# Kernel tuning notes

Hardware: AMD Instinct MI355X
Metric: run time of the kernel (lower is better)

Reference implementation:

```python
import jax, jax.numpy as jnp
import numpy as np

V, E, HID, D = 10000, 512, 512, 14
FEAT = 512  # attention feature dim (== C)


def setup_inputs() -> dict:
    key = jax.random.key(0)
    ks = jax.random.split(key, 20)
    s = 0.02
    inp = {
        "features": jax.random.normal(ks[0], (32, 512, 7, 7), jnp.float32),
        "captions": jax.random.randint(ks[1], (32, 60), 0, V),
        "disease": jax.random.uniform(ks[2], (32, D), jnp.float32),
        # embedding
        "emb": jax.random.normal(ks[3], (V, E), jnp.float32) * s,
        # attention: attn Linear(feat+hid -> hid), v Linear(hid -> 1)
        "W_attn": jax.random.normal(ks[4], (FEAT + HID, HID), jnp.float32) * s,
        "b_attn": jnp.zeros((HID,), jnp.float32),
        "W_v": jax.random.normal(ks[5], (HID, 1), jnp.float32) * s,
        "b_v": jnp.zeros((1,), jnp.float32),
        # attention disease_proj: 14->128->512
        "W_dp1": jax.random.normal(ks[6], (D, 128), jnp.float32) * s,
        "b_dp1": jnp.zeros((128,), jnp.float32),
        "W_dp2": jax.random.normal(ks[7], (128, HID), jnp.float32) * s,
        "b_dp2": jnp.zeros((HID,), jnp.float32),
        # disease_encoder: 14->128->256 (dropout = identity at eval)
        "W_de1": jax.random.normal(ks[8], (D, 128), jnp.float32) * s,
        "b_de1": jnp.zeros((128,), jnp.float32),
        "W_de2": jax.random.normal(ks[9], (128, 256), jnp.float32) * s,
        "b_de2": jnp.zeros((256,), jnp.float32),
        # LSTM (input = E + 512 + 256 = 1280), gate order i,f,g,o
        "W_ih": jax.random.normal(ks[10], (E + FEAT + 256, 4 * HID), jnp.float32) * s,
        "W_hh": jax.random.normal(ks[11], (HID, 4 * HID), jnp.float32) * s,
        "b_ih": jnp.zeros((4 * HID,), jnp.float32),
        "b_hh": jnp.zeros((4 * HID,), jnp.float32),
        # fc: hid -> vocab
        "W_fc": jax.random.normal(ks[12], (HID, V), jnp.float32) * s,
        "b_fc": jnp.zeros((V,), jnp.float32),
    }
    return inp


def reference(features, captions, disease, emb, W_attn, b_attn, W_v, b_v,
              W_dp1, b_dp1, W_dp2, b_dp2, W_de1, b_de1, W_de2, b_de2,
              W_ih, W_hh, b_ih, b_hh, W_fc, b_fc):
    B, C = features.shape[0], features.shape[1]
    f = features.reshape(B, C, -1).transpose(0, 2, 1)  # [B, N, 512]

    embs = emb[captions]  # [B, T, E]

    # time-invariant disease contexts
    dis_ctx = jax.nn.relu(disease @ W_de1 + b_de1) @ W_de2 + b_de2   # [B,256]
    dis_att = jax.nn.relu(disease @ W_dp1 + b_dp1) @ W_dp2 + b_dp2  # [B,HID]

    # split attn weight: energy = tanh(f@Wf + (h+dis_att)@Wh + b)
    Wf, Wh = W_attn[:FEAT], W_attn[FEAT:]
    f_proj = jnp.einsum('bnf,fh->bnh', f, Wf)  # precompute feature part

    def step(carry, emb_t):
        h, c = carry  # [B,HID] each
        hid = h + dis_att
        energy = jnp.tanh(f_proj + (hid @ Wh + b_attn)[:, None, :])  # [B,N,HID]
        scores = (energy @ W_v).squeeze(-1) + b_v[0]                 # [B,N]
        alpha = jax.nn.softmax(scores, axis=1)
        context = jnp.einsum('bn,bnf->bf', alpha, f)                 # [B,512]
        x = jnp.concatenate([emb_t, context, dis_ctx], axis=1)       # [B,1280]
        gates = x @ W_ih + h @ W_hh + b_ih + b_hh
        i, fg, g, o = jnp.split(gates, 4, axis=1)
        c_new = jax.nn.sigmoid(fg) * c + jax.nn.sigmoid(i) * jnp.tanh(g)
        h_new = jax.nn.sigmoid(o) * jnp.tanh(c_new)
        return (h_new, c_new), h_new

    h0 = jnp.zeros((B, HID), f.dtype)
    c0 = jnp.zeros((B, HID), f.dtype)
    _, h_seq = jax.lax.scan(step, (h0, c0), embs.transpose(1, 0, 2))  # [T,B,HID]

    logits = h_seq @ W_fc + b_fc          # [T,B,V]
    return logits.transpose(1, 0, 2)      # [B,T,V]
```

## Files before the change

### kernel.cpp

```cpp
#include <hip/hip_runtime.h>
#include <math.h>

#define BB 32
#define NP 49
#define FE 512
#define HI 512
#define EM 512
#define TT 60
#define G4 2048
#define NV 10000
#define ND 14
#define NBLK 80

typedef __attribute__((ext_vector_type(8))) short short8v;
typedef __attribute__((ext_vector_type(4))) float float4v;

__device__ __forceinline__ float fsig(float x){ return 1.0f/(1.0f+__expf(-x)); }
__device__ __forceinline__ float ftanh(float x){
    x = fminf(fmaxf(x, -15.0f), 15.0f);
    float e = __expf(2.0f*x);
    return (e-1.0f)/(e+1.0f);
}
__device__ __forceinline__ ushort f2bf(float x){
    union { float f; unsigned u; } v; v.f = x;
    unsigned r = v.u + 0x7fff + ((v.u >> 16) & 1);
    return (ushort)(r >> 16);
}
__device__ __forceinline__ float bf2f(ushort h){
    union { float f; unsigned u; } v; v.u = ((unsigned)h) << 16;
    return v.f;
}
__device__ __forceinline__ ushort f2bf_trunc(float x){
    return (ushort)(__float_as_uint(x) >> 16);
}

__global__ void k_transpose(const float* __restrict__ feat, float* __restrict__ fT){
    int b = blockIdx.y;
    int cb = blockIdx.x * 64;
    __shared__ float tile[64][NP+1];
    const float* src = feat + (size_t)b*FE*NP;
    for (int idx = threadIdx.x; idx < 64*NP; idx += 256){
        int cl = idx / NP, n = idx % NP;
        tile[cl][n] = src[(size_t)(cb+cl)*NP + n];
    }
    __syncthreads();
    float* dst = fT + (size_t)b*NP*FE;
    for (int idx = threadIdx.x; idx < 64*NP; idx += 256){
        int cl = idx % 64, n = idx / 64;
        dst[(size_t)n*FE + cb + cl] = tile[cl][n];
    }
}

__global__ void k_disease(const float* __restrict__ dis,
                          const float* __restrict__ Wdp1, const float* __restrict__ bdp1,
                          const float* __restrict__ Wdp2, const float* __restrict__ bdp2,
                          const float* __restrict__ Wde1, const float* __restrict__ bde1,
                          const float* __restrict__ Wde2, const float* __restrict__ bde2,
                          const float* __restrict__ Wattn, const float* __restrict__ battn,
                          const float* __restrict__ Wih, const float* __restrict__ bih,
                          const float* __restrict__ bhh,
                          float* __restrict__ daw, float* __restrict__ disWih){
    int b = blockIdx.x;
    int tid = threadIdx.x;
    __shared__ float d[ND];
    __shared__ float hp[128], he[128];
    __shared__ float datt[HI];
    __shared__ float dctx[256];
    if (tid < ND) d[tid] = dis[b*ND + tid];
    __syncthreads();
    if (tid < 128){
        float accP = bdp1[tid], accE = bde1[tid];
        for (int k=0;k<ND;k++){ accP += d[k]*Wdp1[k*128+tid]; accE += d[k]*Wde1[k*128+tid]; }
        hp[tid] = fmaxf(accP, 0.f);
        he[tid] = fmaxf(accE, 0.f);
    }
    __syncthreads();
    for (int j = tid; j < HI; j += 256){
        float a = bdp2[j];
        for (int k=0;k<128;k++) a += hp[k]*Wdp2[k*HI+j];
        datt[j] = a;
    }
    if (tid < 256){
        float a = bde2[tid];
        for (int k=0;k<128;k++) a += he[k]*Wde2[k*256+tid];
        dctx[tid] = a;
    }
    __syncthreads();
    for (int j = tid; j < HI; j += 256){
        float a = battn[j];
        for (int k=0;k<HI;k++) a += datt[k]*Wattn[(size_t)(FE+k)*HI + j];
        daw[b*HI + j] = a;
    }
    for (int j = tid; j < G4; j += 256){
        float a = bih[j] + bhh[j];
        for (int k=0;k<256;k++) a += dctx[k]*Wih[(size_t)(EM+FE+k)*G4 + j];
        disWih[b*G4 + j] = a;
    }
}

__device__ __forceinline__ void stage_rows32(const float* __restrict__ src0, size_t ldsrc,
                                             const int* __restrict__ rowmap,
                                             ushort* h_hi, ushort* h_lo, int tid){
    #pragma unroll
    for (int it = 0; it < 4; it++){
        int flat = (it*512 + tid)*8;
        int row = flat >> 9, k = flat & 511;
        const float* src = src0 + (rowmap ? (size_t)rowmap[row]*ldsrc : (size_t)row*ldsrc) + k;
        float4 v0 = *(const float4*)(src);
        float4 v1 = *(const float4*)(src + 4);
        float fv[8] = {v0.x,v0.y,v0.z,v0.w,v1.x,v1.y,v1.z,v1.w};
        union { ushort u[8]; uint4 v; } ph, pl;
        #pragma unroll
        for (int j = 0; j < 8; j++){
            ushort hi = f2bf(fv[j]);
            ph.u[j] = hi;
            pl.u[j] = f2bf_trunc(fv[j] - bf2f(hi));
        }
        int di = (row*512 + k) ^ ((row&7)<<3);
        *(uint4*)&h_hi[di] = ph.v;
        *(uint4*)&h_lo[di] = pl.v;
    }
}

__device__ __forceinline__ void mfma_32x32(const ushort* h_hi, const ushort* h_lo,
                                           const float* __restrict__ Wb, size_t ldB, int col0,
                                           int lane, float4v acc[2][2]){
    int m = lane & 15, kg = lane >> 4;
    int a0 = m*512 + kg*8;
    int a1 = (16+m)*512 + kg*8;
    int axr = (m&7)<<3;
    for (int ks = 0; ks < 16; ks++){
        short8v ah0 = *(const short8v*)&h_hi[(a0 + ks*32) ^ axr];
        short8v al0 = *(const short8v*)&h_lo[(a0 + ks*32) ^ axr];
        short8v ah1 = *(const short8v*)&h_hi[(a1 + ks*32) ^ axr];
        short8v al1 = *(const short8v*)&h_lo[(a1 + ks*32) ^ axr];
        #pragma unroll
        for (int cj = 0; cj < 2; cj++){
            int v = col0 + cj*16 + m;
            int k0 = ks*32 + kg*8;
            const float* wp = Wb + (size_t)k0*ldB + v;
            float w[8];
            #pragma unroll
            for (int i = 0; i < 8; i++) w[i] = wp[(size_t)i*ldB];
            union { ushort u[8]; short8v s; } bh, bl;
            #pragma unroll
            for (int i = 0; i < 8; i++){
                ushort hi = f2bf(w[i]);
                bh.u[i] = hi;
                bl.u[i] = f2bf_trunc(w[i] - bf2f(hi));
            }
            acc[0][cj] = __builtin_amdgcn_mfma_f32_16x16x32_bf16(ah0, bh.s, acc[0][cj], 0,0,0);
            acc[0][cj] = __builtin_amdgcn_mfma_f32_16x16x32_bf16(al0, bh.s, acc[0][cj], 0,0,0);
            acc[0][cj] = __builtin_amdgcn_mfma_f32_16x16x32_bf16(ah0, bl.s, acc[0][cj], 0,0,0);
            acc[1][cj] = __builtin_amdgcn_mfma_f32_16x16x32_bf16(ah1, bh.s, acc[1][cj], 0,0,0);
            acc[1][cj] = __builtin_amdgcn_mfma_f32_16x16x32_bf16(al1, bh.s, acc[1][cj], 0,0,0);
            acc[1][cj] = __builtin_amdgcn_mfma_f32_16x16x32_bf16(ah1, bl.s, acc[1][cj], 0,0,0);
        }
    }
}

__launch_bounds__(512, 1)
__global__ void k_fproj(const float* __restrict__ fT, const float* __restrict__ Wattn,
                        float* __restrict__ f_proj){
    __shared__ __align__(16) ushort h_hi[16384], h_lo[16384];
    int r0 = blockIdx.x*32, vt = blockIdx.y;
    int tid = threadIdx.x, lane = tid & 63, wave = tid >> 6;
    stage_rows32(fT + (size_t)r0*FE, FE, nullptr, h_hi, h_lo, tid);
    __syncthreads();
    int col0 = vt*256 + wave*32;
    float4v acc[2][2];
    acc[0][0]=(float4v){0,0,0,0}; acc[0][1]=(float4v){0,0,0,0};
    acc[1][0]=(float4v){0,0,0,0}; acc[1][1]=(float4v){0,0,0,0};
    mfma_32x32(h_hi, h_lo, Wattn, HI, col0, lane, acc);
    int m = lane & 15, kg = lane >> 4;
    #pragma unroll
    for (int cj = 0; cj < 2; cj++){
        int col = col0 + cj*16 + m;
        #pragma unroll
        for (int ri = 0; ri < 2; ri++){
            int arow0 = ri*16 + kg*4;
            #pragma unroll
            for (int r = 0; r < 4; r++)
                f_proj[(size_t)(r0 + arow0 + r)*HI + col] = acc[ri][cj][r];
        }
    }
}

__launch_bounds__(512, 1)
__global__ void k_fwc(const float* __restrict__ fT, const float* __restrict__ Wih,
                      float* __restrict__ fWcP){
    __shared__ __align__(16) ushort h_hi[16384], h_lo[16384];
    int r0 = blockIdx.x*32, vt = blockIdx.y;
    int tid = threadIdx.x, lane = tid & 63, wave = tid >> 6;
    stage_rows32(fT + (size_t)r0*FE, FE, nullptr, h_hi, h_lo, tid);
    __syncthreads();
    int col0 = vt*256 + wave*32;
    float4v acc[2][2];
    acc[0][0]=(float4v){0,0,0,0}; acc[0][1]=(float4v){0,0,0,0};
    acc[1][0]=(float4v){0,0,0,0}; acc[1][1]=(float4v){0,0,0,0};
    mfma_32x32(h_hi, h_lo, Wih + (size_t)FE*G4, G4, col0, lane, acc);
    int m = lane & 15, kg = lane >> 4;
    #pragma unroll
    for (int cj = 0; cj < 2; cj++){
        int gc = col0 + cj*16 + m;
        int blk = (gc & 511) >> 3, m8 = gc & 7, g = gc >> 9;
        #pragma unroll
        for (int ri = 0; ri < 2; ri++){
            int arow0 = ri*16 + kg*4;
            #pragma unroll
            for (int r = 0; r < 4; r++){
                int R = r0 + arow0 + r;
                int b = R / 49, n = R - b*49;
                fWcP[(((size_t)blk*BB + b)*NP + n)*32 + m8*4 + g] = acc[ri][cj][r];
            }
        }
    }
}

__launch_bounds__(512, 1)
__global__ void k_preg(const int* __restrict__ caps, const float* __restrict__ emb,
                       const float* __restrict__ Wih, const float* __restrict__ disWih,
                       float* __restrict__ preGP){
    __shared__ __align__(16) ushort h_hi[16384], h_lo[16384];
    __shared__ int bidx[32];
    int r0 = blockIdx.x*32, vt = blockIdx.y;
    int tid = threadIdx.x, lane = tid & 63, wave = tid >> 6;
    if (tid < 32) bidx[tid] = caps[r0 + tid];
    __syncthreads();
    stage_rows32(emb, EM, bidx, h_hi, h_lo, tid);
    __syncthreads();
    int col0 = vt*256 + wave*32;
    float4v acc[2][2];
    acc[0][0]=(float4v){0,0,0,0}; acc[0][1]=(float4v){0,0,0,0};
    acc[1][0]=(float4v){0,0,0,0}; acc[1][1]=(float4v){0,0,0,0};
    mfma_32x32(h_hi, h_lo, Wih, G4, col0, lane, acc);
    int m = lane & 15, kg = lane >> 4;
    #pragma unroll
    for (int cj = 0; cj < 2; cj++){
        int gc = col0 + cj*16 + m;
        int blk = (gc & 511) >> 3, m8 = gc & 7, g = gc >> 9;
        #pragma unroll
        for (int ri = 0; ri < 2; ri++){
            int arow0 = ri*16 + kg*4;
            #pragma unroll
            for (int r = 0; r < 4; r++){
                int R = r0 + arow0 + r;
                int b = R / 60, t = R - b*60;
                preGP[(((size_t)blk*TT + t)*BB + b)*32 + m8*4 + g] =
                    acc[ri][cj][r] + disWih[b*G4 + gc];
            }
        }
    }
}

__device__ __forceinline__ void gridbar(int* bar, int tgt){
    __syncthreads();
    if (threadIdx.x == 0)
        __hip_atomic_store(bar + blockIdx.x*16, tgt, __ATOMIC_RELEASE, __HIP_MEMORY_SCOPE_AGENT);
    if (blockIdx.x == 0 && threadIdx.x < 64){
        int l = threadIdx.x;
        for (;;){
            int v0 = __hip_atomic_load(bar + l*16, __ATOMIC_RELAXED, __HIP_MEMORY_SCOPE_AGENT);
            int v1 = (l < NBLK-64) ? __hip_atomic_load(bar + (64+l)*16, __ATOMIC_RELAXED, __HIP_MEMORY_SCOPE_AGENT) : tgt;
            if (__all(v0 >= tgt && v1 >= tgt)) break;
            __builtin_amdgcn_s_sleep(1);
        }
        if (l < 10)
            __hip_atomic_store(bar + 1536 + l*16, tgt, __ATOMIC_RELEASE, __HIP_MEMORY_SCOPE_AGENT);
    }
    if (threadIdx.x == 0){
        int g = blockIdx.x >> 3;
        while (__hip_atomic_load(bar + 1536 + g*16, __ATOMIC_RELAXED, __HIP_MEMORY_SCOPE_AGENT) < tgt)
            __builtin_amdgcn_s_sleep(1);
    }
    __syncthreads();
}

__launch_bounds__(512, 1)
__global__ void k_scan_coop(const float* __restrict__ f_proj, const float* __restrict__ fWcP,
                            const float* __restrict__ preGP, const float* __restrict__ daw,
                            const float* __restrict__ Wattn, const float* __restrict__ Whh,
                            const float* __restrict__ Wv,
                            float* __restrict__ h_seq, float* __restrict__ a_buf,
                            float* __restrict__ scores, int* __restrict__ bar){
    __shared__ __align__(16) ushort h_hi[16384], h_lo[16384];
    __shared__ __align__(16) ushort w_hi[16384], w_lo[16384];
    __shared__ float al[32*52];
    __shared__ float gbuf[32*33];
    __shared__ float daw_lds[32*32];
    __shared__ float gv[32*36];
    __shared__ float cst[256];
    __shared__ float wvl[512];
    int bk = blockIdx.x;
    int tid = threadIdx.x;
    int lane = tid & 63, wave = tid >> 6;
    bool isGate = bk < 64;

    {
        int k = tid;
        if (isGate){
            const float* wr = Whh + (size_t)k*G4 + bk*8;
            #pragma unroll
            for (int g = 0; g < 4; g++){
                float4 v0 = *(const float4*)(wr + g*512);
                float4 v1 = *(const float4*)(wr + g*512 + 4);
                float vv[8] = {v0.x,v0.y,v0.z,v0.w,v1.x,v1.y,v1.z,v1.w};
                #pragma unroll
                for (int u = 0; u < 8; u++){
                    int c = u*4 + g;
                    ushort hi = f2bf(vv[u]);
                    ushort lo = f2bf(vv[u] - bf2f(hi));
                    int idx = (c*512 + k) ^ ((c&7)<<3);
                    w_hi[idx] = hi; w_lo[idx] = lo;
                }
            }
        } else {
            const float* wr = Wattn + (size_t)(FE + k)*HI + (bk-64)*32;
            #pragma unroll
            for (int cq = 0; cq < 8; cq++){
                float4 v = *(const float4*)(wr + cq*4);
                float vv[4] = {v.x,v.y,v.z,v.w};
                #pragma unroll
                for (int q = 0; q < 4; q++){
                    int c = cq*4 + q;
                    ushort hi = f2bf(vv[q]);
                    ushort lo = f2bf(vv[q] - bf2f(hi));
                    int idx = (c*512 + k) ^ ((c&7)<<3);
                    w_hi[idx] = hi; w_lo[idx] = lo;
                }
            }
            for (int i = tid; i < 1024; i += 512){
                int b = i >> 5, c = i & 31;
                daw_lds[i] = daw[b*HI + (bk-64)*32 + c];
            }
        }
        if (tid < 256) cst[tid] = 0.f;
        wvl[tid] = Wv[tid];
    }
    __syncthreads();

    int tgt = 0;
    for (int t = 0; t < TT; t++){
        if (t == 0){
            uint4 z = make_uint4(0,0,0,0);
            #pragma unroll
            for (int it = 0; it < 4; it++){
                int flat = (it*512 + tid)*8;
                int b = flat >> 9, k = flat & 511;
                int di = (b*512 + k) ^ ((b&7)<<3);
                *(uint4*)&h_hi[di] = z;
                *(uint4*)&h_lo[di] = z;
            }
        } else {
            const float* hs = h_seq + (size_t)(t-1)*BB*HI;
            #pragma unroll
            for (int it = 0; it < 4; it++){
                int flat = (it*512 + tid)*8;
                int b = flat >> 9, k = flat & 511;
                float4 v0 = *(const float4*)(hs + flat);
                float4 v1 = *(const float4*)(hs + flat + 4);
                float fv[8] = {v0.x,v0.y,v0.z,v0.w,v1.x,v1.y,v1.z,v1.w};
                union { ushort u[8]; uint4 v; } ph, pl;
                #pragma unroll
                for (int j = 0; j < 8; j++){
                    ushort hi = f2bf(fv[j]);
                    ph.u[j] = hi;
                    pl.u[j] = f2bf(fv[j] - bf2f(hi));
                }
                int di = (b*512 + k) ^ ((b&7)<<3);
                *(uint4*)&h_hi[di] = ph.v;
                *(uint4*)&h_lo[di] = pl.v;
            }
        }
        __syncthreads();

        if (wave < 4){
            int rbase = (wave >> 1) * 16, cbase = (wave & 1) * 16;
            int m = lane & 15, kg = lane >> 4;
            int arow = rbase + m, bcol = cbase + m;
            int abase = arow*512 + kg*8, axr = (arow&7)<<3;
            int bbase = bcol*512 + kg*8, bxr = (bcol&7)<<3;
            float4v acc = {0.f,0.f,0.f,0.f};
            #pragma unroll
            for (int ks = 0; ks < 16; ks++){
                int ai = (abase + ks*32) ^ axr;
                int bi = (bbase + ks*32) ^ bxr;
                short8v ahi = *(const short8v*)&h_hi[ai];
                short8v alo = *(const short8v*)&h_lo[ai];
                short8v bhi = *(const short8v*)&w_hi[bi];
                short8v blo = *(const short8v*)&w_lo[bi];
                acc = __builtin_amdgcn_mfma_f32_16x16x32_bf16(ahi, bhi, acc, 0,0,0);
                acc = __builtin_amdgcn_mfma_f32_16x16x32_bf16(alo, bhi, acc, 0,0,0);
                acc = __builtin_amdgcn_mfma_f32_16x16x32_bf16(ahi, blo, acc, 0,0,0);
            }
            int ccol = cbase + (lane & 15);
            int crow0 = rbase + (lane >> 4)*4;
            if (isGate){
                #pragma unroll
                for (int r = 0; r < 4; r++)
                    gbuf[(crow0+r)*33 + ccol] = acc[r];
            } else {
                int cb = (bk-64)*32;
                float* ab = a_buf + (size_t)t*BB*HI;
                #pragma unroll
                for (int r = 0; r < 4; r++)
                    ab[(size_t)(crow0+r)*HI + cb + ccol] = acc[r] + daw_lds[(crow0+r)*32 + ccol];
            }
        }
        gridbar(bar, ++tgt);

        {
            int wid = tid >> 6, l = tid & 63;
            for (int p = bk + wid*NBLK; p < BB*NP; p += NBLK*8){
                int pb = p / NP, pn = p - pb*NP;
                const float* fpn = f_proj + ((size_t)pb*NP + pn)*HI;
                const float* at  = a_buf + ((size_t)t*BB + pb)*HI;
                int j = l*8;
                float4 f0 = *(const float4*)(fpn + j);
                float4 a0 = *(const float4*)(at + j);
                float4 f1 = *(const float4*)(fpn + j + 4);
                float4 a1 = *(const float4*)(at + j + 4);
                float s = wvl[j+0]*ftanh(f0.x + a0.x)
                        + wvl[j+1]*ftanh(f0.y + a0.y)
                        + wvl[j+2]*ftanh(f0.z + a0.z)
                        + wvl[j+3]*ftanh(f0.w + a0.w)
                        + wvl[j+4]*ftanh(f1.x + a1.x)
                        + wvl[j+5]*ftanh(f1.y + a1.y)
                        + wvl[j+6]*ftanh(f1.z + a1.z)
                        + wvl[j+7]*ftanh(f1.w + a1.w);
                #pragma unroll
                for (int off = 32; off; off >>= 1) s += __shfl_xor(s, off);
                if (l == 0) scores[t*(BB*NP) + p] = s;
            }
        }
        gridbar(bar, ++tgt);

        if (isGate){
            int hw = tid >> 5, l32 = tid & 31;
            #pragma unroll
            for (int rep = 0; rep < 2; rep++){
                int b = hw + rep*16;
                const float* sb = scores + t*(BB*NP) + b*NP;
                float s0 = sb[l32];
                float s1 = (l32 < 17) ? sb[32 + l32] : -1e30f;
                float m = fmaxf(s0, s1);
                #pragma unroll
                for (int off = 16; off; off >>= 1) m = fmaxf(m, __shfl_xor(m, off, 32));
                float e0 = __expf(s0 - m);
                float e1 = (l32 < 17) ? __expf(s1 - m) : 0.f;
                float sm = e0 + e1;
                #pragma unroll
                for (int off = 16; off; off >>= 1) sm += __shfl_xor(sm, off, 32);
                float inv = 1.f / sm;
                al[b*52 + l32] = e0*inv;
                if (l32 < 17) al[b*52 + 32 + l32] = e1*inv;
            }
            __syncthreads();
            {
                int b = tid >> 4, cp = tid & 15;
                float g0 = gbuf[b*33 + cp];
                float g1 = gbuf[b*33 + cp + 16];
                const float* pgp = preGP + (((size_t)bk*TT + t)*BB + b)*32;
                g0 += pgp[cp];
                g1 += pgp[cp + 16];
                const float* fw = fWcP + (((size_t)bk*BB + b)*NP)*32;
                for (int n = 0; n < NP; n++){
                    float av = al[b*52 + n];
                    g0 += av*fw[n*32 + cp];
                    g1 += av*fw[n*32 + cp + 16];
                }
                gv[b*36 + cp]      = g0;
                gv[b*36 + cp + 16] = g1;
            }
            __syncthreads();
            if (tid < 256){
                int b = tid >> 3, m = tid & 7;
                float gi = gv[b*36 + m*4 + 0];
                float gf = gv[b*36 + m*4 + 1];
                float gg = gv[b*36 + m*4 + 2];
                float go = gv[b*36 + m*4 + 3];
                float cn = fsig(gf)*cst[b*8 + m] + fsig(gi)*ftanh(gg);
                float hn = fsig(go)*ftanh(cn);
                cst[b*8 + m] = cn;
                h_seq[(size_t)t*BB*HI + b*HI + bk*8 + m] = hn;
            }
        }
        gridbar(bar, ++tgt);
    }
}

__launch_bounds__(512, 1)
__global__ void k_logits(const float* __restrict__ h_seq, const float* __restrict__ Wfc,
                         const float* __restrict__ bfc, float* __restrict__ out){
    __shared__ __align__(16) ushort h_hi[32768], h_lo[32768];
    int t0 = blockIdx.x*2, vt = blockIdx.y;
    int tid = threadIdx.x, lane = tid & 63, wave = tid >> 6;
    const float* hs = h_seq + (size_t)t0*BB*HI;
    #pragma unroll
    for (int it = 0; it < 8; it++){
        int flat = (it*512 + tid)*8;
        int row = flat >> 9, k = flat & 511;
        float4 v0 = *(const float4*)(hs + flat);
        float4 v1 = *(const float4*)(hs + flat + 4);
        float fv[8] = {v0.x,v0.y,v0.z,v0.w,v1.x,v1.y,v1.z,v1.w};
        union { ushort u[8]; uint4 v; } ph, pl;
        #pragma unroll
        for (int j = 0; j < 8; j++){
            ushort hi = f2bf(fv[j]);
            ph.u[j] = hi;
            pl.u[j] = f2bf_trunc(fv[j] - bf2f(hi));
        }
        int di = (row*512 + k) ^ ((row&7)<<3);
        *(uint4*)&h_hi[di] = ph.v;
        *(uint4*)&h_lo[di] = pl.v;
    }
    __syncthreads();

    int m = lane & 15, kg = lane >> 4;
    int cb = vt*256 + wave*32;
    int ab[4];
    #pragma unroll
    for (int rg = 0; rg < 4; rg++) ab[rg] = (rg*16 + m)*512 + kg*8;
    int axr = (m&7)<<3;
    float4v acc[4][2];
    #pragma unroll
    for (int rg = 0; rg < 4; rg++){ acc[rg][0]=(float4v){0,0,0,0}; acc[rg][1]=(float4v){0,0,0,0}; }
    const short8v bz = {0,0,0,0,0,0,0,0};

    for (int ks = 0; ks < 16; ks++){
        short8v ah[4], al[4];
        #pragma unroll
        for (int rg = 0; rg < 4; rg++){
            int ai = (ab[rg] + ks*32) ^ axr;
            ah[rg] = *(const short8v*)&h_hi[ai];
            al[rg] = *(const short8v*)&h_lo[ai];
        }
        #pragma unroll
        for (int cj = 0; cj < 2; cj++){
            int v = cb + cj*16 + m;
            short8v bhi = bz, blo = bz;
            if (v < NV){
                int k0 = ks*32 + kg*8;
                const float* wp = Wfc + (size_t)k0*NV + v;
                float w[8];
                #pragma unroll
                for (int i = 0; i < 8; i++) w[i] = wp[(size_t)i*NV];
                union { ushort u[8]; short8v s; } bh, bl;
                #pragma unroll
                for (int i = 0; i < 8; i++){
                    ushort hi = f2bf(w[i]);
                    bh.u[i] = hi;
                    bl.u[i] = f2bf_trunc(w[i] - bf2f(hi));
                }
                bhi = bh.s; blo = bl.s;
            }
            #pragma unroll
            for (int rg = 0; rg < 4; rg++){
                acc[rg][cj] = __builtin_amdgcn_mfma_f32_16x16x32_bf16(ah[rg], bhi, acc[rg][cj], 0,0,0);
                acc[rg][cj] = __builtin_amdgcn_mfma_f32_16x16x32_bf16(al[rg], bhi, acc[rg][cj], 0,0,0);
                acc[rg][cj] = __builtin_amdgcn_mfma_f32_16x16x32_bf16(ah[rg], blo, acc[rg][cj], 0,0,0);
            }
        }
    }
    #pragma unroll
    for (int cj = 0; cj < 2; cj++){
        int v = cb + cj*16 + m;
        if (v < NV){
            float bias = bfc[v];
            #pragma unroll
            for (int rg = 0; rg < 4; rg++){
                int t = t0 + (rg >> 1);
                int b0 = (rg & 1)*16 + kg*4;
                #pragma unroll
                for (int r = 0; r < 4; r++)
                    out[((size_t)(b0+r)*TT + t)*NV + v] = acc[rg][cj][r] + bias;
            }
        }
    }
}

extern "C" void kernel_launch(void* const* d_in, const int* in_sizes, int n_in,
                              void* d_out, int out_size, void* d_ws, size_t ws_size,
                              hipStream_t stream){
    const float* features = (const float*)d_in[0];
    const int*   captions = (const int*)d_in[1];
    const float* disease  = (const float*)d_in[2];
    const float* emb      = (const float*)d_in[3];
    const float* W_attn   = (const float*)d_in[4];
    const float* b_attn   = (const float*)d_in[5];
    const float* W_v      = (const float*)d_in[6];
    const float* W_dp1    = (const float*)d_in[8];
    const float* b_dp1    = (const float*)d_in[9];
    const float* W_dp2    = (const float*)d_in[10];
    const float* b_dp2    = (const float*)d_in[11];
    const float* W_de1    = (const float*)d_in[12];
    const float* b_de1    = (const float*)d_in[13];
    const float* W_de2    = (const float*)d_in[14];
    const float* b_de2    = (const float*)d_in[15];
    const float* W_ih     = (const float*)d_in[16];
    const float* W_hh     = (const float*)d_in[17];
    const float* b_ih     = (const float*)d_in[18];
    const float* b_hh     = (const float*)d_in[19];
    const float* W_fc     = (const float*)d_in[20];
    const float* b_fc     = (const float*)d_in[21];
    float* out = (float*)d_out;

    const size_t N_HSEQ = (size_t)TT*BB*HI;
    float* h_seq = (float*)d_ws;
    int*   bar   = (int*)((char*)d_ws + N_HSEQ*sizeof(float));

    const size_t N_FT   = (size_t)BB*NP*FE;
    const size_t N_FP   = (size_t)BB*NP*HI;
    const size_t N_FWC  = (size_t)BB*NP*G4;
    const size_t N_PREG = (size_t)BB*TT*G4;
    const size_t N_ABUF = (size_t)TT*BB*HI;
    const size_t N_SC   = (size_t)TT*BB*NP;
    float* fT     = out;
    float* f_proj = fT + N_FT;
    float* fWcP   = f_proj + N_FP;
    float* preGP  = fWcP + N_FWC;
    float* a_buf  = preGP + N_PREG;
    float* scores = a_buf + N_ABUF;
    float* disWih = scores + N_SC;
    float* daw    = disWih + (size_t)BB*G4;

    hipMemsetAsync(bar, 0, 8192, stream);
    k_transpose<<<dim3(8,BB),256,0,stream>>>(features, fT);
    k_disease<<<BB,256,0,stream>>>(disease, W_dp1,b_dp1,W_dp2,b_dp2,
                                   W_de1,b_de1,W_de2,b_de2,
                                   W_attn,b_attn, W_ih,b_ih,b_hh,
                                   daw, disWih);
    k_fproj<<<dim3(49,2),512,0,stream>>>(fT, W_attn, f_proj);
    k_fwc<<<dim3(49,8),512,0,stream>>>(fT, W_ih, fWcP);
    k_preg<<<dim3(60,8),512,0,stream>>>(captions, emb, W_ih, disWih, preGP);
    k_scan_coop<<<NBLK,512,0,stream>>>(f_proj, fWcP, preGP, daw,
                                       W_attn, W_hh, W_v,
                                       h_seq, a_buf, scores, bar);
    k_logits<<<dim3(TT/2,40),512,0,stream>>>(h_seq, W_fc, b_fc, out);
}
```

Measured before the change: 1.693 ms.

## Fuse attention scoring into attn blocks, drop one grid barrier per step

Each of the 16 attention blocks now computes partial attention scores for its own 32 hidden columns using a column-blocked f_proj layout kept local. The partial scores go to a per-block buffer that the gate blocks sum before the softmax. This removes the a_buf round trip and one of the two grid barriers per timestep. The barrier itself is also simplified to packed flags and a single release word, which trades cache-line padding for fewer stores and may add contention. Each gate block now does a 16-way reduction over the partial scores, and the attention blocks carry more tanh work per block.

```diff
diff --git a/kernel.cpp b/kernel.cpp
--- a/kernel.cpp
+++ b/kernel.cpp
@@ -11,6 +11,7 @@
 #define NV 10000
 #define ND 14
 #define NBLK 80
+#define NPAIR (BB*NP)
 
 typedef __attribute__((ext_vector_type(8))) short short8v;
 typedef __attribute__((ext_vector_type(4))) float float4v;
@@ -161,7 +162,7 @@
 
 __launch_bounds__(512, 1)
 __global__ void k_fproj(const float* __restrict__ fT, const float* __restrict__ Wattn,
-                        float* __restrict__ f_proj){
+                        float* __restrict__ f_projB){
     __shared__ __align__(16) ushort h_hi[16384], h_lo[16384];
     int r0 = blockIdx.x*32, vt = blockIdx.y;
     int tid = threadIdx.x, lane = tid & 63, wave = tid >> 6;
@@ -176,12 +177,13 @@
     #pragma unroll
     for (int cj = 0; cj < 2; cj++){
         int col = col0 + cj*16 + m;
+        int bkA = col >> 5, c = col & 31;
         #pragma unroll
         for (int ri = 0; ri < 2; ri++){
             int arow0 = ri*16 + kg*4;
             #pragma unroll
             for (int r = 0; r < 4; r++)
-                f_proj[(size_t)(r0 + arow0 + r)*HI + col] = acc[ri][cj][r];
+                f_projB[((size_t)bkA*NPAIR + (r0 + arow0 + r))*32 + c] = acc[ri][cj][r];
         }
     }
 }
@@ -256,45 +258,45 @@
 __device__ __forceinline__ void gridbar(int* bar, int tgt){
     __syncthreads();
     if (threadIdx.x == 0)
-        __hip_atomic_store(bar + blockIdx.x*16, tgt, __ATOMIC_RELEASE, __HIP_MEMORY_SCOPE_AGENT);
+        __hip_atomic_store(bar + blockIdx.x, tgt, __ATOMIC_RELEASE, __HIP_MEMORY_SCOPE_AGENT);
     if (blockIdx.x == 0 && threadIdx.x < 64){
         int l = threadIdx.x;
         for (;;){
-            int v0 = __hip_atomic_load(bar + l*16, __ATOMIC_RELAXED, __HIP_MEMORY_SCOPE_AGENT);
-            int v1 = (l < NBLK-64) ? __hip_atomic_load(bar + (64+l)*16, __ATOMIC_RELAXED, __HIP_MEMORY_SCOPE_AGENT) : tgt;
+            int v0 = __hip_atomic_load(bar + l, __ATOMIC_RELAXED, __HIP_MEMORY_SCOPE_AGENT);
+            int v1 = (l < NBLK-64) ? __hip_atomic_load(bar + 64 + l, __ATOMIC_RELAXED, __HIP_MEMORY_SCOPE_AGENT) : tgt;
             if (__all(v0 >= tgt && v1 >= tgt)) break;
             __builtin_amdgcn_s_sleep(1);
         }
-        if (l < 10)
-            __hip_atomic_store(bar + 1536 + l*16, tgt, __ATOMIC_RELEASE, __HIP_MEMORY_SCOPE_AGENT);
+        if (l == 0)
+            __hip_atomic_store(bar + 128, tgt, __ATOMIC_RELEASE, __HIP_MEMORY_SCOPE_AGENT);
     }
     if (threadIdx.x == 0){
-        int g = blockIdx.x >> 3;
-        while (__hip_atomic_load(bar + 1536 + g*16, __ATOMIC_RELAXED, __HIP_MEMORY_SCOPE_AGENT) < tgt)
+        while (__hip_atomic_load(bar + 128, __ATOMIC_RELAXED, __HIP_MEMORY_SCOPE_AGENT) < tgt)
             __builtin_amdgcn_s_sleep(1);
     }
     __syncthreads();
 }
 
 __launch_bounds__(512, 1)
-__global__ void k_scan_coop(const float* __restrict__ f_proj, const float* __restrict__ fWcP,
+__global__ void k_scan_coop(const float* __restrict__ f_projB, const float* __restrict__ fWcP,
                             const float* __restrict__ preGP, const float* __restrict__ daw,
                             const float* __restrict__ Wattn, const float* __restrict__ Whh,
                             const float* __restrict__ Wv,
-                            float* __restrict__ h_seq, float* __restrict__ a_buf,
-                            float* __restrict__ scores, int* __restrict__ bar){
+                            float* __restrict__ h_seq, float* __restrict__ scoresP,
+                            int* __restrict__ bar){
     __shared__ __align__(16) ushort h_hi[16384], h_lo[16384];
     __shared__ __align__(16) ushort w_hi[16384], w_lo[16384];
     __shared__ float al[32*52];
     __shared__ float gbuf[32*33];
-    __shared__ float daw_lds[32*32];
+    __shared__ float uni[NPAIR];
     __shared__ float gv[32*36];
     __shared__ float cst[256];
-    __shared__ float wvl[512];
+    __shared__ float wvl[32];
     int bk = blockIdx.x;
     int tid = threadIdx.x;
     int lane = tid & 63, wave = tid >> 6;
     bool isGate = bk < 64;
+    int bkA = bk - 64;
 
     {
         int k = tid;
@@ -315,7 +317,7 @@
                 }
             }
         } else {
-            const float* wr = Wattn + (size_t)(FE + k)*HI + (bk-64)*32;
+            const float* wr = Wattn + (size_t)(FE + k)*HI + bkA*32;
             #pragma unroll
             for (int cq = 0; cq < 8; cq++){
                 float4 v = *(const float4*)(wr + cq*4);
@@ -331,11 +333,11 @@
             }
             for (int i = tid; i < 1024; i += 512){
                 int b = i >> 5, c = i & 31;
-                daw_lds[i] = daw[b*HI + (bk-64)*32 + c];
-            }
+                uni[i] = daw[b*HI + bkA*32 + c];
+            }
+            if (tid < 32) wvl[tid] = Wv[bkA*32 + tid];
         }
         if (tid < 256) cst[tid] = 0.f;
-        wvl[tid] = Wv[tid];
     }
     __syncthreads();
 
@@ -400,77 +402,90 @@
                 for (int r = 0; r < 4; r++)
                     gbuf[(crow0+r)*33 + ccol] = acc[r];
             } else {
-                int cb = (bk-64)*32;
-                float* ab = a_buf + (size_t)t*BB*HI;
                 #pragma unroll
                 for (int r = 0; r < 4; r++)
-                    ab[(size_t)(crow0+r)*HI + cb + ccol] = acc[r] + daw_lds[(crow0+r)*32 + ccol];
-            }
+                    gbuf[(crow0+r)*33 + ccol] = acc[r] + uni[(crow0+r)*32 + ccol];
+            }
+        }
+        __syncthreads();
+
+        float g0r = 0.f, g1r = 0.f;
+        if (!isGate){
+            const float* fB = f_projB + (size_t)bkA*NPAIR*32;
+            float* spt = scoresP + ((size_t)t*16 + bkA)*NPAIR;
+            #pragma unroll
+            for (int it = 0; it < 4; it++){
+                int p = it*512 + tid;
+                if (p < NPAIR){
+                    int pb = (int)((unsigned)p/49u);
+                    const float* ga = &gbuf[pb*33];
+                    const float4* f4 = (const float4*)(fB + (size_t)p*32);
+                    float s = 0.f;
+                    #pragma unroll
+                    for (int c4 = 0; c4 < 8; c4++){
+                        float4 fv = f4[c4];
+                        int c = c4*4;
+                        s += wvl[c+0]*ftanh(fv.x + ga[c+0])
+                           + wvl[c+1]*ftanh(fv.y + ga[c+1])
+                           + wvl[c+2]*ftanh(fv.z + ga[c+2])
+                           + wvl[c+3]*ftanh(fv.w + ga[c+3]);
+                    }
+                    spt[p] = s;
+                }
+            }
+        } else {
+            int b = tid >> 4, cp = tid & 15;
+            const float* pgp = preGP + (((size_t)bk*TT + t)*BB + b)*32;
+            g0r = gbuf[b*33 + cp] + pgp[cp];
+            g1r = gbuf[b*33 + cp + 16] + pgp[cp + 16];
         }
         gridbar(bar, ++tgt);
 
-        {
-            int wid = tid >> 6, l = tid & 63;
-            for (int p = bk + wid*NBLK; p < BB*NP; p += NBLK*8){
-                int pb = p / NP, pn = p - pb*NP;
-                const float* fpn = f_proj + ((size_t)pb*NP + pn)*HI;
-                const float* at  = a_buf + ((size_t)t*BB + pb)*HI;
-                int j = l*8;
-                float4 f0 = *(const float4*)(fpn + j);
-                float4 a0 = *(const float4*)(at + j);
-                float4 f1 = *(const float4*)(fpn + j + 4);
-                float4 a1 = *(const float4*)(at + j + 4);
-                float s = wvl[j+0]*ftanh(f0.x + a0.x)
-                        + wvl[j+1]*ftanh(f0.y + a0.y)
-                        + wvl[j+2]*ftanh(f0.z + a0.z)
-                        + wvl[j+3]*ftanh(f0.w + a0.w)
-                        + wvl[j+4]*ftanh(f1.x + a1.x)
-                        + wvl[j+5]*ftanh(f1.y + a1.y)
-                        + wvl[j+6]*ftanh(f1.z + a1.z)
-                        + wvl[j+7]*ftanh(f1.w + a1.w);
-                #pragma unroll
-                for (int off = 32; off; off >>= 1) s += __shfl_xor(s, off);
-                if (l == 0) scores[t*(BB*NP) + p] = s;
-            }
-        }
-        gridbar(bar, ++tgt);
-
         if (isGate){
-            int hw = tid >> 5, l32 = tid & 31;
-            #pragma unroll
-            for (int rep = 0; rep < 2; rep++){
-                int b = hw + rep*16;
-                const float* sb = scores + t*(BB*NP) + b*NP;
-                float s0 = sb[l32];
-                float s1 = (l32 < 17) ? sb[32 + l32] : -1e30f;
-                float m = fmaxf(s0, s1);
-                #pragma unroll
-                for (int off = 16; off; off >>= 1) m = fmaxf(m, __shfl_xor(m, off, 32));
-                float e0 = __expf(s0 - m);
-                float e1 = (l32 < 17) ? __expf(s1 - m) : 0.f;
-                float sm = e0 + e1;
-                #pragma unroll
-                for (int off = 16; off; off >>= 1) sm += __shfl_xor(sm, off, 32);
-                float inv = 1.f / sm;
-                al[b*52 + l32] = e0*inv;
-                if (l32 < 17) al[b*52 + 32 + l32] = e1*inv;
+            const float* spt = scoresP + (size_t)t*16*NPAIR;
+            #pragma unroll
+            for (int it = 0; it < 4; it++){
+                int p = it*512 + tid;
+                if (p < NPAIR){
+                    float s = 0.f;
+                    #pragma unroll
+                    for (int k2 = 0; k2 < 16; k2++) s += spt[(size_t)k2*NPAIR + p];
+                    uni[p] = s;
+                }
+            }
+            __syncthreads();
+            {
+                int hw = tid >> 5, l32 = tid & 31;
+                #pragma unroll
+                for (int rep = 0; rep < 2; rep++){
+                    int b = hw + rep*16;
+                    const float* sb = uni + b*NP;
+                    float s0 = sb[l32];
+                    float s1 = (l32 < 17) ? sb[32 + l32] : -1e30f;
+                    float m = fmaxf(s0, s1);
+                    #pragma unroll
+                    for (int off = 16; off; off >>= 1) m = fmaxf(m, __shfl_xor(m, off, 32));
+                    float e0 = __expf(s0 - m);
+                    float e1 = (l32 < 17) ? __expf(s1 - m) : 0.f;
+                    float sm = e0 + e1;
+                    #pragma unroll
+                    for (int off = 16; off; off >>= 1) sm += __shfl_xor(sm, off, 32);
+                    float inv = 1.f / sm;
+                    al[b*52 + l32] = e0*inv;
+                    if (l32 < 17) al[b*52 + 32 + l32] = e1*inv;
+                }
             }
             __syncthreads();
             {
                 int b = tid >> 4, cp = tid & 15;
-                float g0 = gbuf[b*33 + cp];
-                float g1 = gbuf[b*33 + cp + 16];
-                const float* pgp = preGP + (((size_t)bk*TT + t)*BB + b)*32;
-                g0 += pgp[cp];
-                g1 += pgp[cp + 16];
                 const float* fw = fWcP + (((size_t)bk*BB + b)*NP)*32;
                 for (int n = 0; n < NP; n++){
                     float av = al[b*52 + n];
-                    g0 += av*fw[n*32 + cp];
-                    g1 += av*fw[n*32 + cp + 16];
-                }
-                gv[b*36 + cp]      = g0;
-                gv[b*36 + cp + 16] = g1;
+                    g0r += av*fw[n*32 + cp];
+                    g1r += av*fw[n*32 + cp + 16];
+                }
+                gv[b*36 + cp]      = g0r;
+                gv[b*36 + cp + 16] = g1r;
             }
             __syncthreads();
             if (tid < 256){
@@ -610,31 +625,29 @@
     int*   bar   = (int*)((char*)d_ws + N_HSEQ*sizeof(float));
 
     const size_t N_FT   = (size_t)BB*NP*FE;
-    const size_t N_FP   = (size_t)BB*NP*HI;
+    const size_t N_FPB  = (size_t)16*NPAIR*32;
     const size_t N_FWC  = (size_t)BB*NP*G4;
     const size_t N_PREG = (size_t)BB*TT*G4;
-    const size_t N_ABUF = (size_t)TT*BB*HI;
-    const size_t N_SC   = (size_t)TT*BB*NP;
+    const size_t N_SCP  = (size_t)TT*16*NPAIR;
     float* fT     = out;
-    float* f_proj = fT + N_FT;
-    float* fWcP   = f_proj + N_FP;
+    float* f_projB= fT + N_FT;
+    float* fWcP   = f_projB + N_FPB;
     float* preGP  = fWcP + N_FWC;
-    float* a_buf  = preGP + N_PREG;
-    float* scores = a_buf + N_ABUF;
-    float* disWih = scores + N_SC;
+    float* scoresP= preGP + N_PREG;
+    float* disWih = scoresP + N_SCP;
     float* daw    = disWih + (size_t)BB*G4;
 
-    hipMemsetAsync(bar, 0, 8192, stream);
+    hipMemsetAsync(bar, 0, 1024, stream);
     k_transpose<<<dim3(8,BB),256,0,stream>>>(features, fT);
     k_disease<<<BB,256,0,stream>>>(disease, W_dp1,b_dp1,W_dp2,b_dp2,
                                    W_de1,b_de1,W_de2,b_de2,
                                    W_attn,b_attn, W_ih,b_ih,b_hh,
                                    daw, disWih);
-    k_fproj<<<dim3(49,2),512,0,stream>>>(fT, W_attn, f_proj);
+    k_fproj<<<dim3(49,2),512,0,stream>>>(fT, W_attn, f_projB);
     k_fwc<<<dim3(49,8),512,0,stream>>>(fT, W_ih, fWcP);
     k_preg<<<dim3(60,8),512,0,stream>>>(captions, emb, W_ih, disWih, preGP);
-    k_scan_coop<<<NBLK,512,0,stream>>>(f_proj, fWcP, preGP, daw,
+    k_scan_coop<<<NBLK,512,0,stream>>>(f_projB, fWcP, preGP, daw,
                                        W_attn, W_hh, W_v,
-                                       h_seq, a_buf, scores, bar);
+                                       h_seq, scoresP, bar);
     k_logits<<<dim3(TT/2,40),512,0,stream>>>(h_seq, W_fc, b_fc, out);
 }
```

Result: slower. 2.227 ms (+31.5%).
